# Optimization experiments

Hardware: AMD Instinct MI355X
Metric: run time of the kernel (lower is better)

Reference implementation:

```python
import jax, jax.numpy as jnp
import numpy as np

K = 20
EPS = 1e-5


def _knn_idx(pts, k):
    # pts: [B,N,C] -> [B,N,k] indices of k nearest neighbors (self included),
    # matching torch topk on negative squared distance.
    inner = jnp.einsum('bnc,bmc->bnm', pts, pts)
    sq = jnp.sum(pts * pts, axis=-1)
    neg_dist = 2.0 * inner - sq[:, :, None] - sq[:, None, :]  # [B,N,N]
    return jax.lax.top_k(neg_dist, k)[1]


def _graph_feature(pts, k):
    # pts: [B,N,C] -> edge features [B,N,k,2C] = concat(neighbor-center, center)
    idx = _knn_idx(pts, k)                       # [B,N,k]
    nb = jax.vmap(lambda p, i: p[i])(pts, idx)   # gather: [B,N,k,C]
    ctr = jnp.broadcast_to(pts[:, :, None, :], nb.shape)
    return jnp.concatenate([nb - ctr, ctr], axis=-1)


def _bn(x, g, b, axes):
    # BatchNorm with batch statistics (torch training-mode forward)
    m = jnp.mean(x, axes, keepdims=True)
    v = jnp.var(x, axes, keepdims=True)
    return (x - m) * jax.lax.rsqrt(v + EPS) * g + b


def _edge_block(pts, W, b, g, beta):
    # EdgeConv: graph feature -> 1x1 conv (matmul over channels) -> BN -> ReLU -> max over k
    f = _graph_feature(pts, K)                       # [B,N,k,2C]
    h = jnp.einsum('bnkc,oc->bnko', f, W) + b        # 1x1 conv
    h = jax.nn.relu(_bn(h, g, beta, (0, 1, 2)))
    return jnp.max(h, axis=2)                        # [B,N,O]


def _forward(x, conv1_w, conv1_b, bn1_g, bn1_b, conv2_w, conv2_b, bn2_g, bn2_b,
             conv3_w, conv3_b, bn3_g, bn3_b, conv4_w, conv4_b, bn4_g, bn4_b,
             fc1_w, fc1_b, bnf1_g, bnf1_b, fc2_w, fc2_b, bnf2_g, bnf2_b,
             fc3_w, fc3_b, bnf3_g, bnf3_b, fc4_w, fc4_b):
    pts = x[:, 0]  # squeeze(1): [B,N,3] (channels-last == torch [B,3,N] transposed)
    x1 = _edge_block(pts, conv1_w, conv1_b, bn1_g, bn1_b)   # [B,N,64]
    x2 = _edge_block(x1, conv2_w, conv2_b, bn2_g, bn2_b)    # [B,N,64]
    x3 = _edge_block(x2, conv3_w, conv3_b, bn3_g, bn3_b)    # [B,N,128]
    x4 = _edge_block(x3, conv4_w, conv4_b, bn4_g, bn4_b)    # [B,N,256]
    # maxpool over all N points (kernel (crop_point_num,1))
    x_64 = jnp.max(x2, axis=1)    # [B,64]
    x_128 = jnp.max(x3, axis=1)   # [B,128]
    x_256 = jnp.max(x4, axis=1)   # [B,256]
    h = jnp.concatenate([x_256, x_128, x_64], axis=1)  # [B,448]
    h = jax.nn.relu(_bn(h @ fc1_w.T + fc1_b, bnf1_g, bnf1_b, (0,)))
    h = jax.nn.relu(_bn(h @ fc2_w.T + fc2_b, bnf2_g, bnf2_b, (0,)))
    h = jax.nn.relu(_bn(h @ fc3_w.T + fc3_b, bnf3_g, bnf3_b, (0,)))
    return h @ fc4_w.T + fc4_b    # [B,1]


def setup_inputs() -> dict:
    key = jax.random.key(0)
    ks = jax.random.split(key, 16)
    B, N = 8, 2048
    f32 = jnp.float32

    def w(k, shape):
        return jax.random.normal(k, shape, f32) / np.float32(np.sqrt(shape[-1]))

    def bn_params(c):
        return jnp.ones((c,), f32), jnp.zeros((c,), f32)

    bn1_g, bn1_b = bn_params(64)
    bn2_g, bn2_b = bn_params(64)
    bn3_g, bn3_b = bn_params(128)
    bn4_g, bn4_b = bn_params(256)
    bnf1_g, bnf1_b = bn_params(256)
    bnf2_g, bnf2_b = bn_params(128)
    bnf3_g, bnf3_b = bn_params(16)
    return {
        'x': jax.random.normal(ks[0], (B, 1, N, 3), f32),
        'conv1_w': w(ks[1], (64, 6)),   'conv1_b': jnp.zeros((64,), f32),
        'bn1_g': bn1_g, 'bn1_b': bn1_b,
        'conv2_w': w(ks[2], (64, 128)), 'conv2_b': jnp.zeros((64,), f32),
        'bn2_g': bn2_g, 'bn2_b': bn2_b,
        'conv3_w': w(ks[3], (128, 128)), 'conv3_b': jnp.zeros((128,), f32),
        'bn3_g': bn3_g, 'bn3_b': bn3_b,
        'conv4_w': w(ks[4], (256, 256)), 'conv4_b': jnp.zeros((256,), f32),
        'bn4_g': bn4_g, 'bn4_b': bn4_b,
        'fc1_w': w(ks[5], (256, 448)), 'fc1_b': jnp.zeros((256,), f32),
        'bnf1_g': bnf1_g, 'bnf1_b': bnf1_b,
        'fc2_w': w(ks[6], (128, 256)), 'fc2_b': jnp.zeros((128,), f32),
        'bnf2_g': bnf2_g, 'bnf2_b': bnf2_b,
        'fc3_w': w(ks[7], (16, 128)), 'fc3_b': jnp.zeros((16,), f32),
        'bnf3_g': bnf3_g, 'bnf3_b': bnf3_b,
        'fc4_w': w(ks[8], (1, 16)), 'fc4_b': jnp.zeros((1,), f32),
    }


def reference(x, conv1_w, conv1_b, bn1_g, bn1_b, conv2_w, conv2_b, bn2_g, bn2_b,
              conv3_w, conv3_b, bn3_g, bn3_b, conv4_w, conv4_b, bn4_g, bn4_b,
              fc1_w, fc1_b, bnf1_g, bnf1_b, fc2_w, fc2_b, bnf2_g, bnf2_b,
              fc3_w, fc3_b, bnf3_g, bnf3_b, fc4_w, fc4_b):
    return _forward(x, conv1_w, conv1_b, bn1_g, bn1_b, conv2_w, conv2_b, bn2_g, bn2_b,
                    conv3_w, conv3_b, bn3_g, bn3_b, conv4_w, conv4_b, bn4_g, bn4_b,
                    fc1_w, fc1_b, bnf1_g, bnf1_b, fc2_w, fc2_b, bnf2_g, bnf2_b,
                    fc3_w, fc3_b, bnf3_g, bnf3_b, fc4_w, fc4_b)
```

## Files before the change

### kernel.cpp

```cpp
#include <hip/hip_runtime.h>
#include <hip/hip_bf16.h>
#include <cfloat>

constexpr int BATCH = 8, NPTS = 2048, KNN = 20;
constexpr int NROWS = BATCH * NPTS;
constexpr float EPSV = 1e-5f;
constexpr int SB = 256;
constexpr int PR = 64;
constexpr int RBB = NPTS / 16;
constexpr int KC2 = 48;
constexpr int QCAP = 512;
constexpr int NCH = 4;

using u16 = unsigned short;
using u64 = unsigned long long;
typedef __attribute__((ext_vector_type(8))) short short8;
typedef __attribute__((ext_vector_type(4))) float f32x4;

__global__ void diag_kernel(float* out, float v) {
    if (threadIdx.x < 8) out[threadIdx.x] = v;
}

__global__ __launch_bounds__(256) void fill_zero_kernel(float* __restrict__ p, int n) {
    int i = blockIdx.x * 256 + threadIdx.x;
    if (i < n) p[i] = 0.f;
}

template<int C>
__global__ __launch_bounds__(256) void sqnorm_kernel(const float* __restrict__ X,
                                                     float* __restrict__ sq) {
    int r = blockIdx.x * 256 + threadIdx.x;
    const float* x = X + (size_t)r * C;
    float s = 0.f;
#pragma unroll
    for (int c = 0; c < C; ++c) { float v = x[c]; s = fmaf(v, v, s); }
    sq[r] = s;
}

template<int C>
__global__ __launch_bounds__(256) void split_pack_kernel(const float* __restrict__ X,
                                                         u16* __restrict__ XPH,
                                                         u16* __restrict__ XPL) {
    constexpr int KB = C / 32;
    int e = blockIdx.x * 256 + threadIdx.x;
    int lane = e & 63;
    int rest = e >> 6;
    int kb = rest % KB;
    int Rb = rest / KB;
    int row = Rb * 16 + (lane & 15);
    int col = kb * 32 + (lane >> 4) * 8;
    const float* src = &X[(size_t)row * C + col];
    u16 h[8], l[8];
#pragma unroll
    for (int q = 0; q < 8; ++q) {
        float v = src[q];
        __hip_bfloat16 hb = __float2bfloat16(v);
        float hf = __bfloat162float(hb);
        __hip_bfloat16 lb = __float2bfloat16(v - hf);
        h[q] = *(u16*)&hb; l[q] = *(u16*)&lb;
    }
    u16* dh = &XPH[(size_t)e * 8];
    u16* dl = &XPL[(size_t)e * 8];
#pragma unroll
    for (int q = 0; q < 8; ++q) { dh[q] = h[q]; dl[q] = l[q]; }
}

template<int C, int O>
__global__ __launch_bounds__(256) void wsplit_pack_kernel(const float* __restrict__ W,
                                                          u16* __restrict__ WPH,
                                                          u16* __restrict__ WPL) {
    constexpr int KB = C / 32;
    constexpr int NFRAG = (2 * O / 16) * KB * 64;
    int e = blockIdx.x * 256 + threadIdx.x;
    if (e >= NFRAG) return;
    int lane = e & 63;
    int rest = e >> 6;
    int kb = rest % KB;
    int Nb = rest / KB;
    int n = Nb * 16 + (lane & 15);
    int col = kb * 32 + (lane >> 4) * 8;
    u16 h[8], l[8];
#pragma unroll
    for (int q = 0; q < 8; ++q) {
        int c = col + q;
        float wv = (n < O) ? W[(size_t)n * (2 * C) + c]
                           : W[(size_t)(n - O) * (2 * C) + C + c] - W[(size_t)(n - O) * (2 * C) + c];
        __hip_bfloat16 hb = __float2bfloat16(wv);
        float hf = __bfloat162float(hb);
        __hip_bfloat16 lb = __float2bfloat16(wv - hf);
        h[q] = *(u16*)&hb; l[q] = *(u16*)&lb;
    }
    u16* dh = &WPH[(size_t)e * 8];
    u16* dl = &WPL[(size_t)e * 8];
#pragma unroll
    for (int q = 0; q < 8; ++q) { dh[q] = h[q]; dl[q] = l[q]; }
}

__device__ __forceinline__ float bitonic64_desc_f32(float key, int lane) {
#pragma unroll
    for (int k = 2; k <= 64; k <<= 1) {
#pragma unroll
        for (int j = k >> 1; j > 0; j >>= 1) {
            float p = __shfl_xor(key, j);
            bool keepMax = (((lane & j) == 0) == ((lane & k) == 0));
            key = ((key > p) == keepMax) ? key : p;
        }
    }
    return key;
}

__device__ __forceinline__ u64 bitonic64_desc_u64(u64 key, int lane) {
#pragma unroll
    for (int k = 2; k <= 64; k <<= 1) {
#pragma unroll
        for (int j = k >> 1; j > 0; j >>= 1) {
            u64 p = __shfl_xor(key, j);
            bool keepMax = (((lane & j) == 0) == ((lane & k) == 0));
            key = ((key > p) == keepMax) ? key : p;
        }
    }
    return key;
}

template<int C>
__global__ __launch_bounds__(256) void dist_gemm_kernel(const float* __restrict__ X,
                                                        float* __restrict__ D, int b0) {
    constexpr int KC = (C < 32) ? C : 32;
    __shared__ __align__(16) float As[KC][68];
    __shared__ __align__(16) float Bs[KC][68];
    int b = b0 + blockIdx.z;
    int i0 = blockIdx.y * 64, j0 = blockIdx.x * 64;
    const float* Xb = X + (size_t)b * NPTS * C;
    int tx = threadIdx.x & 15, ty = threadIdx.x >> 4;
    float acc[4][4] = {};
    for (int c0 = 0; c0 < C; c0 += KC) {
        for (int t = threadIdx.x; t < 64 * KC; t += 256) {
            int i = t / KC, c = t % KC;
            As[c][i] = Xb[(size_t)(i0 + i) * C + c0 + c];
            Bs[c][i] = Xb[(size_t)(j0 + i) * C + c0 + c];
        }
        __syncthreads();
#pragma unroll
        for (int c = 0; c < KC; ++c) {
            const float4 av = *(const float4*)&As[c][ty * 4];
            const float4 bv = *(const float4*)&Bs[c][tx * 4];
            float ar[4] = {av.x, av.y, av.z, av.w};
            float br[4] = {bv.x, bv.y, bv.z, bv.w};
#pragma unroll
            for (int r = 0; r < 4; ++r)
#pragma unroll
                for (int q = 0; q < 4; ++q) acc[r][q] = fmaf(ar[r], br[q], acc[r][q]);
        }
        __syncthreads();
    }
    float* Dz = D + (size_t)blockIdx.z * NPTS * NPTS;
#pragma unroll
    for (int r = 0; r < 4; ++r) {
        float4 o4 = make_float4(acc[r][0], acc[r][1], acc[r][2], acc[r][3]);
        *(float4*)&Dz[(size_t)(i0 + ty * 4 + r) * NPTS + j0 + tx * 4] = o4;
    }
}

__global__ __launch_bounds__(256) void topk_kernel(const float* __restrict__ D,
                                                   const float* __restrict__ sq,
                                                   u16* __restrict__ idx_out, int b0) {
    __shared__ u64 qkey[4][QCAP];
    __shared__ int qn[4];
    int b = b0 + blockIdx.z;
    int w = threadIdx.x >> 6, lane = threadIdx.x & 63;
    int i = blockIdx.x * 4 + w;
    const float* Drow = D + ((size_t)blockIdx.z * NPTS + i) * NPTS;
    const float* sqb = sq + b * NPTS;
    float sqi = sqb[i];
    if (lane == 0) qn[w] = 0;

    float vals[32];
    float mx = -FLT_MAX;
#pragma unroll
    for (int t = 0; t < 8; ++t) {
        int j = t * 256 + lane * 4;
        float4 v4 = *(const float4*)&Drow[j];
        float4 s4 = *(const float4*)&sqb[j];
        float a0 = (2.f * v4.x - sqi - s4.x) + 0.f;
        float a1 = (2.f * v4.y - sqi - s4.y) + 0.f;
        float a2 = (2.f * v4.z - sqi - s4.z) + 0.f;
        float a3 = (2.f * v4.w - sqi - s4.w) + 0.f;
        vals[t * 4 + 0] = a0; vals[t * 4 + 1] = a1;
        vals[t * 4 + 2] = a2; vals[t * 4 + 3] = a3;
        mx = fmaxf(mx, fmaxf(fmaxf(a0, a1), fmaxf(a2, a3)));
    }

    float sm = bitonic64_desc_f32(mx, lane);
    float T0 = __shfl(sm, 19);

#pragma unroll
    for (int t = 0; t < 32; ++t) {
        float v = vals[t];
        if (v >= T0) {
            unsigned j = (unsigned)((t >> 2) * 256 + lane * 4 + (t & 3));
            unsigned bu = __float_as_uint(v);
            unsigned u = (bu & 0x80000000u) ? ~bu : (bu | 0x80000000u);
            u64 key = ((u64)u << 32) | (u64)(0xFFFFFFFFu - j);
            int slot = atomicAdd(&qn[w], 1);
            if (slot < QCAP) qkey[w][slot] = key;
        }
    }
    int C = qn[w];
    if (C > QCAP) C = QCAP;

    u64 key = (lane < C) ? qkey[w][lane] : 0ull;
    key = bitonic64_desc_u64(key, lane);
    int base = 64;
    while (base < C) {
        if (lane >= 20) {
            int src = base + (lane - 20);
            key = (src < C) ? qkey[w][src] : 0ull;
        }
        key = bitonic64_desc_u64(key, lane);
        base += 44;
    }
    if (lane < 20) {
        unsigned j = 0xFFFFFFFFu - (unsigned)(key & 0xFFFFFFFFull);
        idx_out[(size_t)(b * NPTS + i) * KNN + lane] = (u16)j;
    }
}

template<int C>
__global__ __launch_bounds__(256) void knn_kernel(const u16* __restrict__ XPH,
                                                  const u16* __restrict__ XPL,
                                                  const float* __restrict__ SQ,
                                                  u64* __restrict__ CAND) {
    constexpr int KB = C / 32;
    __shared__ float Dl[16][516];
    __shared__ u64 cand[16][KC2];
    __shared__ int cnt[16];
    int b = blockIdx.z;
    int chunk = blockIdx.x;
    int i0 = blockIdx.y * 16;
    int w = threadIdx.x >> 6, lane = threadIdx.x & 63;
    int l15 = lane & 15, g = lane >> 4;
    size_t base = (size_t)b * RBB * KB * 512;
    const float* sqb = SQ + b * NPTS;

    if (threadIdx.x < 16) cnt[threadIdx.x] = 0;

    int Rba = i0 / 16;
    short8 ahi[KB], alo[KB];
#pragma unroll
    for (int kb = 0; kb < KB; ++kb) {
        size_t ia = base + ((size_t)(Rba * KB + kb) * 64 + lane) * 8;
        ahi[kb] = *(const short8*)&XPH[ia];
        alo[kb] = *(const short8*)&XPL[ia];
    }
    float sqr[4];
#pragma unroll
    for (int r = 0; r < 4; ++r) sqr[r] = sqb[i0 + g * 4 + r];

#pragma unroll
    for (int t = 0; t < 8; ++t) {
        int c = w + 4 * t;
        int Cb = chunk * 32 + c;
        f32x4 acc = {0.f, 0.f, 0.f, 0.f};
#pragma unroll
        for (int kb = 0; kb < KB; ++kb) {
            size_t ib = base + ((size_t)(Cb * KB + kb) * 64 + lane) * 8;
            short8 bhi = *(const short8*)&XPH[ib];
            short8 blo = *(const short8*)&XPL[ib];
            acc = __builtin_amdgcn_mfma_f32_16x16x32_bf16(ahi[kb], bhi, acc, 0, 0, 0);
            acc = __builtin_amdgcn_mfma_f32_16x16x32_bf16(ahi[kb], blo, acc, 0, 0, 0);
            acc = __builtin_amdgcn_mfma_f32_16x16x32_bf16(alo[kb], bhi, acc, 0, 0, 0);
        }
        int colg = Cb * 16 + l15;
        float sqc = sqb[colg];
        int cl = c * 16 + l15;
#pragma unroll
        for (int r = 0; r < 4; ++r)
            Dl[g * 4 + r][cl] = (2.f * acc[r] - sqr[r] - sqc) + 0.f;
    }
    __syncthreads();

    for (int rr = 0; rr < 4; ++rr) {
        int row = w * 4 + rr;
        float vv[8];
        float mx = -FLT_MAX;
#pragma unroll
        for (int q = 0; q < 8; ++q) {
            vv[q] = Dl[row][lane + 64 * q];
            mx = fmaxf(mx, vv[q]);
        }
        float sv = bitonic64_desc_f32(mx, lane);
        float T = __shfl(sv, 19);
#pragma unroll
        for (int q = 0; q < 8; ++q) {
            float v = vv[q];
            if (v >= T) {
                unsigned colg = (unsigned)(chunk * 512 + lane + 64 * q);
                unsigned bu = __float_as_uint(v);
                unsigned u = (bu & 0x80000000u) ? ~bu : (bu | 0x80000000u);
                u64 key = ((u64)u << 32) | (u64)(0xFFFFFFFFu - colg);
                int slot = atomicAdd(&cnt[row], 1);
                if (slot < KC2) cand[row][slot] = key;
            }
        }
        int Cn = cnt[row]; if (Cn > KC2) Cn = KC2;
        u64 key = (lane < Cn) ? cand[row][lane] : 0ull;
        key = bitonic64_desc_u64(key, lane);
        if (lane < 20)
            CAND[(((size_t)(b * NPTS + i0 + row)) * NCH + chunk) * 20 + lane] = key;
    }
}

__global__ __launch_bounds__(256) void knn_merge_kernel(const u64* __restrict__ CAND,
                                                        u16* __restrict__ idx_out) {
    int b = blockIdx.z;
    int w = threadIdx.x >> 6, lane = threadIdx.x & 63;
    int i = blockIdx.x * 4 + w;
    size_t rb = ((size_t)(b * NPTS + i)) * (NCH * 20);
    u64 key = CAND[rb + lane];
    key = bitonic64_desc_u64(key, lane);
    u64 extra = (lane >= 20 && lane < 36) ? CAND[rb + 64 + (lane - 20)] : 0ull;
    if (lane >= 20) key = extra;
    key = bitonic64_desc_u64(key, lane);
    if (lane < 20) {
        unsigned j = 0xFFFFFFFFu - (unsigned)(key & 0xFFFFFFFFull);
        idx_out[((size_t)(b * NPTS + i)) * KNN + lane] = (u16)j;
    }
}

template<int C, int O>
__global__ __launch_bounds__(256) void uvb_mfma_kernel(const u16* __restrict__ XPH,
                                                       const u16* __restrict__ XPL,
                                                       const u16* __restrict__ WPH,
                                                       const u16* __restrict__ WPL,
                                                       const float* __restrict__ bias,
                                                       float* __restrict__ UVA) {
    constexpr int KB = C / 32;
    int b = blockIdx.z;
    int r0 = blockIdx.y * 64, n0 = blockIdx.x * 64;
    int w = threadIdx.x >> 6, lane = threadIdx.x & 63;
    int l15 = lane & 15, g = lane >> 4;
    size_t base = (size_t)b * RBB * KB * 512;
    int Rba = r0 / 16 + w;
    short8 ahi[KB], alo[KB];
#pragma unroll
    for (int kb = 0; kb < KB; ++kb) {
        size_t ia = base + ((size_t)(Rba * KB + kb) * 64 + lane) * 8;
        ahi[kb] = *(const short8*)&XPH[ia];
        alo[kb] = *(const short8*)&XPL[ia];
    }
    float* UVb = UVA + (size_t)b * NPTS * 2 * O;
#pragma unroll
    for (int nt = 0; nt < 4; ++nt) {
        int Nb = n0 / 16 + nt;
        f32x4 acc = {0.f, 0.f, 0.f, 0.f};
#pragma unroll
        for (int kb = 0; kb < KB; ++kb) {
            size_t ib = ((size_t)(Nb * KB + kb) * 64 + lane) * 8;
            short8 bhi = *(const short8*)&WPH[ib];
            short8 blo = *(const short8*)&WPL[ib];
            acc = __builtin_amdgcn_mfma_f32_16x16x32_bf16(ahi[kb], bhi, acc, 0, 0, 0);
            acc = __builtin_amdgcn_mfma_f32_16x16x32_bf16(ahi[kb], blo, acc, 0, 0, 0);
            acc = __builtin_amdgcn_mfma_f32_16x16x32_bf16(alo[kb], bhi, acc, 0, 0, 0);
        }
        int n = n0 + nt * 16 + l15;
        float badd = (n >= O) ? bias[n - O] : 0.f;
        int rbase = r0 + w * 16 + g * 4;
#pragma unroll
        for (int r = 0; r < 4; ++r)
            UVb[(size_t)(rbase + r) * (2 * O) + n] = acc[r] + badd;
    }
}

template<int C, int O>
__global__ __launch_bounds__(256) void uvb_gemm_kernel(const float* __restrict__ X,
                                                       const float* __restrict__ W,
                                                       const float* __restrict__ bias,
                                                       float* __restrict__ UVA) {
    constexpr int KC = (C < 32) ? C : 32;
    __shared__ __align__(16) float As[KC][68];
    __shared__ __align__(16) float Bs[KC][68];
    int b = blockIdx.z;
    int r0 = blockIdx.y * 64, n0 = blockIdx.x * 64;
    int tx = threadIdx.x & 15, ty = threadIdx.x >> 4;
    float acc[4][4] = {};
    for (int c0 = 0; c0 < C; c0 += KC) {
        for (int t = threadIdx.x; t < 64 * KC; t += 256) {
            int i = t / KC, c = t % KC;
            As[c][i] = X[(size_t)(b * NPTS + r0 + i) * C + c0 + c];
            int n = n0 + i;
            float wv;
            if (n < O) wv = W[(size_t)n * (2 * C) + c0 + c];
            else {
                int o = n - O;
                wv = W[(size_t)o * (2 * C) + C + c0 + c] - W[(size_t)o * (2 * C) + c0 + c];
            }
            Bs[c][i] = wv;
        }
        __syncthreads();
#pragma unroll
        for (int c = 0; c < KC; ++c) {
            const float4 av = *(const float4*)&As[c][ty * 4];
            const float4 bv = *(const float4*)&Bs[c][tx * 4];
            float ar[4] = {av.x, av.y, av.z, av.w};
            float br[4] = {bv.x, bv.y, bv.z, bv.w};
#pragma unroll
            for (int r = 0; r < 4; ++r)
#pragma unroll
                for (int q = 0; q < 4; ++q) acc[r][q] = fmaf(ar[r], br[q], acc[r][q]);
        }
        __syncthreads();
    }
    float badd[4] = {0.f, 0.f, 0.f, 0.f};
    if (n0 >= O) {
#pragma unroll
        for (int q = 0; q < 4; ++q) badd[q] = bias[n0 - O + tx * 4 + q];
    }
    float* UVb = UVA + (size_t)b * NPTS * 2 * O;
#pragma unroll
    for (int r = 0; r < 4; ++r) {
        float4 o4 = make_float4(acc[r][0] + badd[0], acc[r][1] + badd[1],
                                acc[r][2] + badd[2], acc[r][3] + badd[3]);
        *(float4*)&UVb[(size_t)(r0 + ty * 4 + r) * (2 * O) + n0 + tx * 4] = o4;
    }
}

template<int O>
__global__ __launch_bounds__(256) void statsb_kernel(const float* __restrict__ UVA,
                                                     const u16* __restrict__ idx,
                                                     float* __restrict__ PART,
                                                     float* __restrict__ HMAX,
                                                     float* __restrict__ HMIN) {
    constexpr int TPR = O / 4;
    constexpr int RPAR = 256 / TPR;
    constexpr int RPB = NPTS / SB;
    __shared__ float sh[256 * 8];
    int b = blockIdx.z;
    const float* UVb = UVA + (size_t)b * NPTS * 2 * O;
    int otid = threadIdx.x % TPR;
    int o = otid * 4;
    int rsub = threadIdx.x / TPR;
    int rbase = blockIdx.x * RPB;
    float s0 = 0, s1 = 0, s2 = 0, s3 = 0, q0 = 0, q1 = 0, q2 = 0, q3 = 0;
    for (int r = rbase + rsub; r < rbase + RPB; r += RPAR) {
        const float4 v4 = *(const float4*)&UVb[(size_t)r * (2 * O) + O + o];
        const u16* ix = idx + (size_t)(b * NPTS + r) * KNN;
        float mx0 = -FLT_MAX, mx1 = -FLT_MAX, mx2 = -FLT_MAX, mx3 = -FLT_MAX;
        float mn0 = FLT_MAX, mn1 = FLT_MAX, mn2 = FLT_MAX, mn3 = FLT_MAX;
#pragma unroll
        for (int k = 0; k < KNN; ++k) {
            int j = (int)ix[k] & (NPTS - 1);
            const float4 u4 = *(const float4*)&UVb[(size_t)j * (2 * O) + o];
            float h0 = u4.x + v4.x, h1 = u4.y + v4.y, h2 = u4.z + v4.z, h3 = u4.w + v4.w;
            s0 += h0; q0 = fmaf(h0, h0, q0); mx0 = fmaxf(mx0, h0); mn0 = fminf(mn0, h0);
            s1 += h1; q1 = fmaf(h1, h1, q1); mx1 = fmaxf(mx1, h1); mn1 = fminf(mn1, h1);
            s2 += h2; q2 = fmaf(h2, h2, q2); mx2 = fmaxf(mx2, h2); mn2 = fminf(mn2, h2);
            s3 += h3; q3 = fmaf(h3, h3, q3); mx3 = fmaxf(mx3, h3); mn3 = fminf(mn3, h3);
        }
        size_t R = (size_t)(b * NPTS + r) * O + o;
        *(float4*)&HMAX[R] = make_float4(mx0, mx1, mx2, mx3);
        *(float4*)&HMIN[R] = make_float4(mn0, mn1, mn2, mn3);
    }
    float* my = &sh[threadIdx.x * 8];
    my[0] = s0; my[1] = s1; my[2] = s2; my[3] = s3;
    my[4] = q0; my[5] = q1; my[6] = q2; my[7] = q3;
    __syncthreads();
    if (threadIdx.x < TPR) {
        float a[8];
#pragma unroll
        for (int c = 0; c < 8; ++c) a[c] = sh[threadIdx.x * 8 + c];
        for (int g = 1; g < RPAR; ++g) {
            const float* p = &sh[(g * TPR + threadIdx.x) * 8];
#pragma unroll
            for (int c = 0; c < 8; ++c) a[c] += p[c];
        }
        float* dst = &PART[((size_t)b * SB + blockIdx.x) * (2 * O)];
#pragma unroll
        for (int c = 0; c < 4; ++c) { dst[o + c] = a[c]; dst[O + o + c] = a[4 + c]; }
    }
}

template<int O>
__global__ __launch_bounds__(256) void part_reduce_kernel(const float* __restrict__ PART,
                                                          float* __restrict__ PART2) {
    constexpr int ROWS = BATCH * SB;
    constexpr int RPG = ROWS / PR;
    int g = blockIdx.x;
    for (int col = threadIdx.x; col < 2 * O; col += 256) {
        float s = 0.f;
        for (int r = 0; r < RPG; ++r)
            s += PART[(size_t)(g * RPG + r) * (2 * O) + col];
        PART2[(size_t)g * (2 * O) + col] = s;
    }
}

template<int O>
__global__ void bnp_kernel(const float* __restrict__ PART2, const float* __restrict__ g,
                           const float* __restrict__ beta, float* __restrict__ bnp) {
    int o = threadIdx.x;
    float s = 0.f, ss = 0.f;
    for (int p = 0; p < PR; ++p) {
        s += PART2[(size_t)p * (2 * O) + o];
        ss += PART2[(size_t)p * (2 * O) + O + o];
    }
    const float cnt = (float)NROWS * (float)KNN;
    float m = s / cnt;
    float var = ss / cnt - m * m;
    float sc = g[o] / sqrtf(var + EPSV);
    bnp[o] = sc;
    bnp[O + o] = beta[o] - m * sc;
}

template<int O>
__global__ __launch_bounds__(256) void applyb_kernel(const float* __restrict__ HMAX,
                                                     const float* __restrict__ HMIN,
                                                     const float* __restrict__ bnp,
                                                     float* __restrict__ Xn) {
    constexpr int TPR = O / 4;
    int e = blockIdx.x * 256 + threadIdx.x;
    int o = (e % TPR) * 4;
    size_t R = (size_t)(e / TPR) * O + o;
    const float4 hx = *(const float4*)&HMAX[R];
    const float4 hn = *(const float4*)&HMIN[R];
    float4 out;
    { float sc = bnp[o + 0], t = bnp[O + o + 0]; out.x = fmaxf(fmaf(sc, (sc >= 0.f) ? hx.x : hn.x, t), 0.f); }
    { float sc = bnp[o + 1], t = bnp[O + o + 1]; out.y = fmaxf(fmaf(sc, (sc >= 0.f) ? hx.y : hn.y, t), 0.f); }
    { float sc = bnp[o + 2], t = bnp[O + o + 2]; out.z = fmaxf(fmaf(sc, (sc >= 0.f) ? hx.z : hn.z, t), 0.f); }
    { float sc = bnp[o + 3], t = bnp[O + o + 3]; out.w = fmaxf(fmaf(sc, (sc >= 0.f) ? hx.w : hn.w, t), 0.f); }
    *(float4*)&Xn[R] = out;
}

__global__ __launch_bounds__(256) void applyb4_kernel(const float* __restrict__ HMAX,
                                                      const float* __restrict__ HMIN,
                                                      const float* __restrict__ bnp,
                                                      float* __restrict__ g0T) {
    constexpr int O = 256;
    constexpr int TPR = O / 4;
    constexpr int RPAR = 256 / TPR;
    constexpr int AB = 32;
    constexpr int RPB = NPTS / AB;
    __shared__ float sh[256 * 4];
    int b = blockIdx.z;
    int otid = threadIdx.x & (TPR - 1);
    int o = otid * 4;
    int rsub = threadIdx.x >> 6;
    int rbase = blockIdx.x * RPB;
    float sc0 = bnp[o + 0], t0 = bnp[O + o + 0];
    float sc1 = bnp[o + 1], t1 = bnp[O + o + 1];
    float sc2 = bnp[o + 2], t2 = bnp[O + o + 2];
    float sc3 = bnp[o + 3], t3 = bnp[O + o + 3];
    float ym0 = 0.f, ym1 = 0.f, ym2 = 0.f, ym3 = 0.f;
    for (int r = rbase + rsub; r < rbase + RPB; r += RPAR) {
        size_t R = (size_t)(b * NPTS + r) * O + o;
        const float4 hx = *(const float4*)&HMAX[R];
        const float4 hn = *(const float4*)&HMIN[R];
        ym0 = fmaxf(ym0, fmaf(sc0, (sc0 >= 0.f) ? hx.x : hn.x, t0));
        ym1 = fmaxf(ym1, fmaf(sc1, (sc1 >= 0.f) ? hx.y : hn.y, t1));
        ym2 = fmaxf(ym2, fmaf(sc2, (sc2 >= 0.f) ? hx.z : hn.z, t2));
        ym3 = fmaxf(ym3, fmaf(sc3, (sc3 >= 0.f) ? hx.w : hn.w, t3));
    }
    float* my = &sh[threadIdx.x * 4];
    my[0] = ym0; my[1] = ym1; my[2] = ym2; my[3] = ym3;
    __syncthreads();
    if (threadIdx.x < TPR) {
        float a0 = ym0, a1 = ym1, a2 = ym2, a3 = ym3;
        for (int g = 1; g < RPAR; ++g) {
            const float* p = &sh[(g * TPR + threadIdx.x) * 4];
            a0 = fmaxf(a0, p[0]); a1 = fmaxf(a1, p[1]);
            a2 = fmaxf(a2, p[2]); a3 = fmaxf(a3, p[3]);
        }
        a0 = fmaxf(a0, 0.f); a1 = fmaxf(a1, 0.f);
        a2 = fmaxf(a2, 0.f); a3 = fmaxf(a3, 0.f);
        atomicMax((int*)&g0T[(o + 0) * 8 + b], __float_as_int(a0));
        atomicMax((int*)&g0T[(o + 1) * 8 + b], __float_as_int(a1));
        atomicMax((int*)&g0T[(o + 2) * 8 + b], __float_as_int(a2));
        atomicMax((int*)&g0T[(o + 3) * 8 + b], __float_as_int(a3));
    }
}

__global__ __launch_bounds__(256) void gmax23_kernel(const float* __restrict__ X2,
                                                     const float* __restrict__ X3,
                                                     float* __restrict__ g0T) {
    int b = blockIdx.x;
    int n0 = blockIdx.y * 32;
    int o = threadIdx.x;
    if (o >= 192) return;
    const float* src; int col, stride, ch;
    if (o < 128) { src = X3; col = o;       stride = 128; ch = 256 + o; }
    else         { src = X2; col = o - 128; stride = 64;  ch = 384 + (o - 128); }
    float m = 0.f;
#pragma unroll 8
    for (int n = n0; n < n0 + 32; ++n)
        m = fmaxf(m, src[((size_t)(b * NPTS + n)) * stride + col]);
    atomicMax((int*)&g0T[ch * 8 + b], __float_as_int(m));
}

__global__ __launch_bounds__(256) void transpose_kernel(const float* __restrict__ w,
                                                        float* __restrict__ wT, int O, int Cc) {
    int e = blockIdx.x * 256 + threadIdx.x;
    if (e >= O * Cc) return;
    int o = e / Cc, c = e - o * Cc;
    wT[c * O + o] = w[e];
}

__global__ __launch_bounds__(64) void fc1_kernel(const float* __restrict__ g0T,
                                                 const float* __restrict__ w1T,
                                                 const float* __restrict__ b1,
                                                 const float* __restrict__ bng,
                                                 const float* __restrict__ bnb,
                                                 float* __restrict__ A) {
    int o = blockIdx.x * 64 + threadIdx.x;
    float acc[8] = {};
    for (int c = 0; c < 448; ++c) {
        float wv = w1T[c * 256 + o];
        const float4 h0 = *(const float4*)&g0T[c * 8];
        const float4 h1 = *(const float4*)&g0T[c * 8 + 4];
        acc[0] = fmaf(wv, h0.x, acc[0]); acc[1] = fmaf(wv, h0.y, acc[1]);
        acc[2] = fmaf(wv, h0.z, acc[2]); acc[3] = fmaf(wv, h0.w, acc[3]);
        acc[4] = fmaf(wv, h1.x, acc[4]); acc[5] = fmaf(wv, h1.y, acc[5]);
        acc[6] = fmaf(wv, h1.z, acc[6]); acc[7] = fmaf(wv, h1.w, acc[7]);
    }
    float bb = b1[o];
    float h[8], m = 0.f;
#pragma unroll
    for (int b = 0; b < 8; ++b) { h[b] = acc[b] + bb; m += h[b]; }
    m *= 0.125f;
    float var = 0.f;
#pragma unroll
    for (int b = 0; b < 8; ++b) { float d = h[b] - m; var = fmaf(d, d, var); }
    var *= 0.125f;
    float sc = bng[o] / sqrtf(var + EPSV);
    float t = bnb[o] - m * sc;
#pragma unroll
    for (int b = 0; b < 8; ++b) A[o * 8 + b] = fmaxf(fmaf(sc, h[b], t), 0.f);
}

__global__ __launch_bounds__(256) void tail_kernel(const float* __restrict__ A,
                                                   const float* __restrict__ w2T, const float* __restrict__ b2,
                                                   const float* __restrict__ g2, const float* __restrict__ be2,
                                                   const float* __restrict__ w3T, const float* __restrict__ b3,
                                                   const float* __restrict__ g3, const float* __restrict__ be3,
                                                   const float* __restrict__ w4, const float* __restrict__ b4,
                                                   float* __restrict__ out) {
    __shared__ __align__(16) float B2[128 * 8];
    __shared__ __align__(16) float C3[16 * 8];
    int tid = threadIdx.x;
    if (tid < 128) {
        int o = tid;
        float acc[8] = {};
        for (int c = 0; c < 256; ++c) {
            float wv = w2T[c * 128 + o];
            const float4 a0 = *(const float4*)&A[c * 8];
            const float4 a1 = *(const float4*)&A[c * 8 + 4];
            acc[0] = fmaf(wv, a0.x, acc[0]); acc[1] = fmaf(wv, a0.y, acc[1]);
            acc[2] = fmaf(wv, a0.z, acc[2]); acc[3] = fmaf(wv, a0.w, acc[3]);
            acc[4] = fmaf(wv, a1.x, acc[4]); acc[5] = fmaf(wv, a1.y, acc[5]);
            acc[6] = fmaf(wv, a1.z, acc[6]); acc[7] = fmaf(wv, a1.w, acc[7]);
        }
        float bb = b2[o];
        float h[8], m = 0.f;
#pragma unroll
        for (int b = 0; b < 8; ++b) { h[b] = acc[b] + bb; m += h[b]; }
        m *= 0.125f;
        float var = 0.f;
#pragma unroll
        for (int b = 0; b < 8; ++b) { float d = h[b] - m; var = fmaf(d, d, var); }
        var *= 0.125f;
        float sc = g2[o] / sqrtf(var + EPSV);
        float t = be2[o] - m * sc;
#pragma unroll
        for (int b = 0; b < 8; ++b) B2[o * 8 + b] = fmaxf(fmaf(sc, h[b], t), 0.f);
    }
    __syncthreads();
    if (tid < 16) {
        int o = tid;
        float acc[8] = {};
        for (int c = 0; c < 128; ++c) {
            float wv = w3T[c * 16 + o];
            const float4 a0 = *(const float4*)&B2[c * 8];
            const float4 a1 = *(const float4*)&B2[c * 8 + 4];
            acc[0] = fmaf(wv, a0.x, acc[0]); acc[1] = fmaf(wv, a0.y, acc[1]);
            acc[2] = fmaf(wv, a0.z, acc[2]); acc[3] = fmaf(wv, a0.w, acc[3]);
            acc[4] = fmaf(wv, a1.x, acc[4]); acc[5] = fmaf(wv, a1.y, acc[5]);
            acc[6] = fmaf(wv, a1.z, acc[6]); acc[7] = fmaf(wv, a1.w, acc[7]);
        }
        float bb = b3[o];
        float h[8], m = 0.f;
#pragma unroll
        for (int b = 0; b < 8; ++b) { h[b] = acc[b] + bb; m += h[b]; }
        m *= 0.125f;
        float var = 0.f;
#pragma unroll
        for (int b = 0; b < 8; ++b) { float d = h[b] - m; var = fmaf(d, d, var); }
        var *= 0.125f;
        float sc = g3[o] / sqrtf(var + EPSV);
        float t = be3[o] - m * sc;
#pragma unroll
        for (int b = 0; b < 8; ++b) C3[o * 8 + b] = fmaxf(fmaf(sc, h[b], t), 0.f);
    }
    __syncthreads();
    if (tid < 8) {
        int b = tid;
        float acc = b4[0];
#pragma unroll
        for (int c = 0; c < 16; ++c) acc = fmaf(w4[c], C3[c * 8 + b], acc);
        out[b] = acc;
    }
}

struct Arena {
    char* base; size_t off, cap; bool ok;
    Arena(void* b, size_t c) : base((char*)b), off(0), cap(c), ok(true) {}
    void* get(size_t bytes) {
        char* p = base + off;
        off += (bytes + 255) & ~(size_t)255;
        if (off > cap) ok = false;
        return p;
    }
};

template<int C, int O>
static void run_stage(const float* Xin, float* Xout, const float* W, const float* bias,
                      const float* g, const float* be, float* SCRBIG, float* UVA,
                      u16* XPH, u16* XPL, u16* WPH, u16* WPL,
                      u16* IDX, float* SQ, float* PART, float* PART2, float* BNP, hipStream_t s) {
    dim3 blk(256);
    float* HMAX = SCRBIG;
    float* HMIN = SCRBIG + (size_t)NROWS * O;
    u64* CANDB = (u64*)SCRBIG;
    sqnorm_kernel<C><<<NROWS / 256, blk, 0, s>>>(Xin, SQ);
    if constexpr (C >= 32) {
        split_pack_kernel<C><<<NROWS * C / 8 / 256, blk, 0, s>>>(Xin, XPH, XPL);
        knn_kernel<C><<<dim3(NCH, NPTS / 16, BATCH), blk, 0, s>>>(XPH, XPL, SQ, CANDB);
        knn_merge_kernel<<<dim3(NPTS / 4, 1, BATCH), blk, 0, s>>>(CANDB, IDX);
        wsplit_pack_kernel<C, O><<<(2 * O * C / 8 + 255) / 256, blk, 0, s>>>(W, WPH, WPL);
        uvb_mfma_kernel<C, O><<<dim3(2 * O / 64, NPTS / 64, BATCH), blk, 0, s>>>(XPH, XPL, WPH, WPL, bias, UVA);
    } else {
        for (int b0 = 0; b0 < BATCH; b0 += 4) {
            dist_gemm_kernel<C><<<dim3(NPTS / 64, NPTS / 64, 4), blk, 0, s>>>(Xin, SCRBIG, b0);
            topk_kernel<<<dim3(NPTS / 4, 1, 4), blk, 0, s>>>(SCRBIG, SQ, IDX, b0);
        }
        uvb_gemm_kernel<C, O><<<dim3(2 * O / 64, NPTS / 64, BATCH), blk, 0, s>>>(Xin, W, bias, UVA);
    }
    statsb_kernel<O><<<dim3(SB, 1, BATCH), blk, 0, s>>>(UVA, IDX, PART, HMAX, HMIN);
    part_reduce_kernel<O><<<PR, blk, 0, s>>>(PART, PART2);
    bnp_kernel<O><<<1, O, 0, s>>>(PART2, g, be, BNP);
    applyb_kernel<O><<<NROWS * (O / 4) / 256, blk, 0, s>>>(HMAX, HMIN, BNP, Xout);
}

static void run_stage4(const float* Xin, const float* W, const float* bias,
                       const float* g, const float* be, float* SCRBIG, float* UVA,
                       u16* XPH, u16* XPL, u16* WPH, u16* WPL,
                       u16* IDX, float* SQ, float* PART, float* PART2, float* BNP, float* G0T,
                       hipStream_t s) {
    constexpr int C = 128;
    dim3 blk(256);
    float* HMAX = SCRBIG;
    float* HMIN = SCRBIG + (size_t)NROWS * 256;
    u64* CANDB = (u64*)SCRBIG;
    sqnorm_kernel<C><<<NROWS / 256, blk, 0, s>>>(Xin, SQ);
    split_pack_kernel<C><<<NROWS * C / 8 / 256, blk, 0, s>>>(Xin, XPH, XPL);
    knn_kernel<C><<<dim3(NCH, NPTS / 16, BATCH), blk, 0, s>>>(XPH, XPL, SQ, CANDB);
    knn_merge_kernel<<<dim3(NPTS / 4, 1, BATCH), blk, 0, s>>>(CANDB, IDX);
    wsplit_pack_kernel<C, 256><<<(512 * C / 8 + 255) / 256, blk, 0, s>>>(W, WPH, WPL);
    uvb_mfma_kernel<C, 256><<<dim3(8, NPTS / 64, BATCH), blk, 0, s>>>(XPH, XPL, WPH, WPL, bias, UVA);
    statsb_kernel<256><<<dim3(SB, 1, BATCH), blk, 0, s>>>(UVA, IDX, PART, HMAX, HMIN);
    part_reduce_kernel<256><<<PR, blk, 0, s>>>(PART, PART2);
    bnp_kernel<256><<<1, 256, 0, s>>>(PART2, g, be, BNP);
    fill_zero_kernel<<<14, blk, 0, s>>>(G0T, 448 * 8);
    applyb4_kernel<<<dim3(32, 1, BATCH), blk, 0, s>>>(HMAX, HMIN, BNP, G0T);
}

extern "C" void kernel_launch(void* const* d_in, const int* in_sizes, int n_in,
                              void* d_out, int out_size, void* d_ws, size_t ws_size,
                              hipStream_t stream) {
    float* out = (float*)d_out;
    if (n_in < 31) { diag_kernel<<<1, 64, 0, stream>>>(out, 9000.f); return; }

    const float* x       = (const float*)d_in[0];
    const float* cw[4]   = {(const float*)d_in[1], (const float*)d_in[5], (const float*)d_in[9],  (const float*)d_in[13]};
    const float* cb[4]   = {(const float*)d_in[2], (const float*)d_in[6], (const float*)d_in[10], (const float*)d_in[14]};
    const float* bg[4]   = {(const float*)d_in[3], (const float*)d_in[7], (const float*)d_in[11], (const float*)d_in[15]};
    const float* bb[4]   = {(const float*)d_in[4], (const float*)d_in[8], (const float*)d_in[12], (const float*)d_in[16]};
    const float* fc1_w = (const float*)d_in[17]; const float* fc1_b = (const float*)d_in[18];
    const float* bnf1_g = (const float*)d_in[19]; const float* bnf1_b = (const float*)d_in[20];
    const float* fc2_w = (const float*)d_in[21]; const float* fc2_b = (const float*)d_in[22];
    const float* bnf2_g = (const float*)d_in[23]; const float* bnf2_b = (const float*)d_in[24];
    const float* fc3_w = (const float*)d_in[25]; const float* fc3_b = (const float*)d_in[26];
    const float* bnf3_g = (const float*)d_in[27]; const float* bnf3_b = (const float*)d_in[28];
    const float* fc4_w = (const float*)d_in[29]; const float* fc4_b = (const float*)d_in[30];

    Arena ar(d_ws, ws_size);
    float* X1 = (float*)ar.get((size_t)NROWS * 64 * 4);
    float* X2 = (float*)ar.get((size_t)NROWS * 64 * 4);
    float* X3 = (float*)ar.get((size_t)NROWS * 128 * 4);
    u16* IDX = (u16*)ar.get((size_t)NROWS * KNN * 2);
    float* SQ = (float*)ar.get((size_t)NROWS * 4);
    float* PART = (float*)ar.get((size_t)BATCH * SB * 512 * 4);
    float* PART2 = (float*)ar.get((size_t)PR * 512 * 4);
    float* BNP = (float*)ar.get(512 * 4);
    float* G0T = (float*)ar.get(448 * 8 * 4);
    float* ABUF = (float*)ar.get(256 * 8 * 4);
    u16* XPH = (u16*)ar.get((size_t)NROWS * 128 * 2);
    u16* XPL = (u16*)ar.get((size_t)NROWS * 128 * 2);
    u16* WPH = (u16*)ar.get(512 * 128 * 2);
    u16* WPL = (u16*)ar.get(512 * 128 * 2);
    float* SCRBIG = (float*)ar.get((size_t)4 * NPTS * NPTS * 4);
    if (!ar.ok) {
        diag_kernel<<<1, 64, 0, stream>>>(out, 3000.f + (float)(ws_size >> 20));
        return;
    }
    float* UVA = SCRBIG + (size_t)2 * NPTS * NPTS;

    dim3 blk(256);
    run_stage<3, 64>(x, X1, cw[0], cb[0], bg[0], bb[0], SCRBIG, UVA, XPH, XPL, WPH, WPL, IDX, SQ, PART, PART2, BNP, stream);
    run_stage<64, 64>(X1, X2, cw[1], cb[1], bg[1], bb[1], SCRBIG, UVA, XPH, XPL, WPH, WPL, IDX, SQ, PART, PART2, BNP, stream);
    run_stage<64, 128>(X2, X3, cw[2], cb[2], bg[2], bb[2], SCRBIG, UVA, XPH, XPL, WPH, WPL, IDX, SQ, PART, PART2, BNP, stream);
    run_stage4(X3, cw[3], cb[3], bg[3], bb[3], SCRBIG, UVA, XPH, XPL, WPH, WPL, IDX, SQ, PART, PART2, BNP, G0T, stream);

    gmax23_kernel<<<dim3(BATCH, 64), blk, 0, stream>>>(X2, X3, G0T);

    float* W1T = SCRBIG;
    float* W2T = W1T + 448 * 256;
    float* W3T = W2T + 256 * 128;
    transpose_kernel<<<(256 * 448 + 255) / 256, blk, 0, stream>>>(fc1_w, W1T, 256, 448);
    transpose_kernel<<<(128 * 256 + 255) / 256, blk, 0, stream>>>(fc2_w, W2T, 128, 256);
    transpose_kernel<<<(16 * 128 + 255) / 256, blk, 0, stream>>>(fc3_w, W3T, 16, 128);
    fc1_kernel<<<4, 64, 0, stream>>>(G0T, W1T, fc1_b, bnf1_g, bnf1_b, ABUF);
    tail_kernel<<<1, 256, 0, stream>>>(ABUF, W2T, fc2_b, bnf2_g, bnf2_b,
                                       W3T, fc3_b, bnf3_g, bnf3_b, fc4_w, fc4_b, out);
}
```

Measured before the change: 718.2 us.

## Fuse stage-1 distance GEMM with top-k and move kNN candidate sorting into merge

For the 3-channel first stage, the separate distance GEMM and top-k kernels are replaced by one kernel. It stages the batch's points and squared norms in shared memory and computes distances on the fly, so the 4×2048×2048 distance matrix is no longer written to and read back from global memory. In the MFMA kNN kernel, candidates above the per-chunk threshold are compacted with ballot/popcount and written straight to global memory with per-chunk counts, instead of being sorted locally through shared-memory atomics; the merge kernel now streams the variable-length lists through bitonic sorts. Risks: the fused kernel caps candidates at 64 where the old one allowed 512, so heavy ties could drop true neighbours, and every block reloads all 2048 points of its batch.

```diff
diff --git a/kernel.cpp b/kernel.cpp
--- a/kernel.cpp
+++ b/kernel.cpp
@@ -9,7 +9,6 @@
 constexpr int PR = 64;
 constexpr int RBB = NPTS / 16;
 constexpr int KC2 = 48;
-constexpr int QCAP = 512;
 constexpr int NCH = 4;
 
 using u16 = unsigned short;
@@ -122,106 +121,57 @@
     return key;
 }
 
-template<int C>
-__global__ __launch_bounds__(256) void dist_gemm_kernel(const float* __restrict__ X,
-                                                        float* __restrict__ D, int b0) {
-    constexpr int KC = (C < 32) ? C : 32;
-    __shared__ __align__(16) float As[KC][68];
-    __shared__ __align__(16) float Bs[KC][68];
-    int b = b0 + blockIdx.z;
-    int i0 = blockIdx.y * 64, j0 = blockIdx.x * 64;
-    const float* Xb = X + (size_t)b * NPTS * C;
-    int tx = threadIdx.x & 15, ty = threadIdx.x >> 4;
-    float acc[4][4] = {};
-    for (int c0 = 0; c0 < C; c0 += KC) {
-        for (int t = threadIdx.x; t < 64 * KC; t += 256) {
-            int i = t / KC, c = t % KC;
-            As[c][i] = Xb[(size_t)(i0 + i) * C + c0 + c];
-            Bs[c][i] = Xb[(size_t)(j0 + i) * C + c0 + c];
-        }
-        __syncthreads();
-#pragma unroll
-        for (int c = 0; c < KC; ++c) {
-            const float4 av = *(const float4*)&As[c][ty * 4];
-            const float4 bv = *(const float4*)&Bs[c][tx * 4];
-            float ar[4] = {av.x, av.y, av.z, av.w};
-            float br[4] = {bv.x, bv.y, bv.z, bv.w};
-#pragma unroll
-            for (int r = 0; r < 4; ++r)
-#pragma unroll
-                for (int q = 0; q < 4; ++q) acc[r][q] = fmaf(ar[r], br[q], acc[r][q]);
-        }
-        __syncthreads();
-    }
-    float* Dz = D + (size_t)blockIdx.z * NPTS * NPTS;
-#pragma unroll
-    for (int r = 0; r < 4; ++r) {
-        float4 o4 = make_float4(acc[r][0], acc[r][1], acc[r][2], acc[r][3]);
-        *(float4*)&Dz[(size_t)(i0 + ty * 4 + r) * NPTS + j0 + tx * 4] = o4;
-    }
-}
-
-__global__ __launch_bounds__(256) void topk_kernel(const float* __restrict__ D,
-                                                   const float* __restrict__ sq,
-                                                   u16* __restrict__ idx_out, int b0) {
-    __shared__ u64 qkey[4][QCAP];
+__global__ __launch_bounds__(256) void topk1_kernel(const float* __restrict__ X,
+                                                    u16* __restrict__ idx_out) {
+    constexpr int Q1 = 64;
+    __shared__ float px[NPTS], py[NPTS], pz[NPTS], sqs[NPTS];
+    __shared__ u64 qkey[4][Q1];
     __shared__ int qn[4];
-    int b = b0 + blockIdx.z;
+    int b = blockIdx.z;
+    const float* Xb = X + (size_t)b * NPTS * 3;
+    for (int k = threadIdx.x; k < NPTS; k += 256) {
+        float xx = Xb[k * 3 + 0], yy = Xb[k * 3 + 1], zz = Xb[k * 3 + 2];
+        px[k] = xx; py[k] = yy; pz[k] = zz;
+        float s = fmaf(xx, xx, 0.f); s = fmaf(yy, yy, s); s = fmaf(zz, zz, s);
+        sqs[k] = s;
+    }
     int w = threadIdx.x >> 6, lane = threadIdx.x & 63;
+    if (lane == 0) qn[w] = 0;
+    __syncthreads();
     int i = blockIdx.x * 4 + w;
-    const float* Drow = D + ((size_t)blockIdx.z * NPTS + i) * NPTS;
-    const float* sqb = sq + b * NPTS;
-    float sqi = sqb[i];
-    if (lane == 0) qn[w] = 0;
-
+    float xi = px[i], yi = py[i], zi = pz[i], sqi = sqs[i];
     float vals[32];
     float mx = -FLT_MAX;
 #pragma unroll
-    for (int t = 0; t < 8; ++t) {
-        int j = t * 256 + lane * 4;
-        float4 v4 = *(const float4*)&Drow[j];
-        float4 s4 = *(const float4*)&sqb[j];
-        float a0 = (2.f * v4.x - sqi - s4.x) + 0.f;
-        float a1 = (2.f * v4.y - sqi - s4.y) + 0.f;
-        float a2 = (2.f * v4.z - sqi - s4.z) + 0.f;
-        float a3 = (2.f * v4.w - sqi - s4.w) + 0.f;
-        vals[t * 4 + 0] = a0; vals[t * 4 + 1] = a1;
-        vals[t * 4 + 2] = a2; vals[t * 4 + 3] = a3;
-        mx = fmaxf(mx, fmaxf(fmaxf(a0, a1), fmaxf(a2, a3)));
-    }
-
+    for (int t = 0; t < 32; ++t) {
+        int j = lane + 64 * t;
+        float d = fmaf(xi, px[j], 0.f);
+        d = fmaf(yi, py[j], d);
+        d = fmaf(zi, pz[j], d);
+        float v = (2.f * d - sqi - sqs[j]) + 0.f;
+        vals[t] = v;
+        mx = fmaxf(mx, v);
+    }
     float sm = bitonic64_desc_f32(mx, lane);
     float T0 = __shfl(sm, 19);
-
 #pragma unroll
     for (int t = 0; t < 32; ++t) {
         float v = vals[t];
         if (v >= T0) {
-            unsigned j = (unsigned)((t >> 2) * 256 + lane * 4 + (t & 3));
+            unsigned j = (unsigned)(lane + 64 * t);
             unsigned bu = __float_as_uint(v);
             unsigned u = (bu & 0x80000000u) ? ~bu : (bu | 0x80000000u);
             u64 key = ((u64)u << 32) | (u64)(0xFFFFFFFFu - j);
             int slot = atomicAdd(&qn[w], 1);
-            if (slot < QCAP) qkey[w][slot] = key;
-        }
-    }
-    int C = qn[w];
-    if (C > QCAP) C = QCAP;
-
-    u64 key = (lane < C) ? qkey[w][lane] : 0ull;
+            if (slot < Q1) qkey[w][slot] = key;
+        }
+    }
+    int Cn = qn[w]; if (Cn > Q1) Cn = Q1;
+    u64 key = (lane < Cn) ? qkey[w][lane] : 0ull;
     key = bitonic64_desc_u64(key, lane);
-    int base = 64;
-    while (base < C) {
-        if (lane >= 20) {
-            int src = base + (lane - 20);
-            key = (src < C) ? qkey[w][src] : 0ull;
-        }
-        key = bitonic64_desc_u64(key, lane);
-        base += 44;
-    }
     if (lane < 20) {
         unsigned j = 0xFFFFFFFFu - (unsigned)(key & 0xFFFFFFFFull);
-        idx_out[(size_t)(b * NPTS + i) * KNN + lane] = (u16)j;
+        idx_out[((size_t)(b * NPTS + i)) * KNN + lane] = (u16)j;
     }
 }
 
@@ -229,11 +179,10 @@
 __global__ __launch_bounds__(256) void knn_kernel(const u16* __restrict__ XPH,
                                                   const u16* __restrict__ XPL,
                                                   const float* __restrict__ SQ,
-                                                  u64* __restrict__ CAND) {
+                                                  u64* __restrict__ CAND,
+                                                  int* __restrict__ CNTS) {
     constexpr int KB = C / 32;
     __shared__ float Dl[16][516];
-    __shared__ u64 cand[16][KC2];
-    __shared__ int cnt[16];
     int b = blockIdx.z;
     int chunk = blockIdx.x;
     int i0 = blockIdx.y * 16;
@@ -242,8 +191,6 @@
     size_t base = (size_t)b * RBB * KB * 512;
     const float* sqb = SQ + b * NPTS;
 
-    if (threadIdx.x < 16) cnt[threadIdx.x] = 0;
-
     int Rba = i0 / 16;
     short8 ahi[KB], alo[KB];
 #pragma unroll
@@ -290,40 +237,55 @@
         }
         float sv = bitonic64_desc_f32(mx, lane);
         float T = __shfl(sv, 19);
+        size_t cb = ((size_t)(b * NPTS + i0 + row) * NCH + chunk) * KC2;
+        int cbase = 0;
 #pragma unroll
         for (int q = 0; q < 8; ++q) {
-            float v = vv[q];
-            if (v >= T) {
-                unsigned colg = (unsigned)(chunk * 512 + lane + 64 * q);
-                unsigned bu = __float_as_uint(v);
-                unsigned u = (bu & 0x80000000u) ? ~bu : (bu | 0x80000000u);
-                u64 key = ((u64)u << 32) | (u64)(0xFFFFFFFFu - colg);
-                int slot = atomicAdd(&cnt[row], 1);
-                if (slot < KC2) cand[row][slot] = key;
+            bool p = vv[q] >= T;
+            u64 mask = __ballot(p);
+            int ofs = __popcll(mask & ((1ull << lane) - 1ull));
+            if (p) {
+                int slot = cbase + ofs;
+                if (slot < KC2) {
+                    unsigned colg = (unsigned)(chunk * 512 + lane + 64 * q);
+                    unsigned bu = __float_as_uint(vv[q]);
+                    unsigned u = (bu & 0x80000000u) ? ~bu : (bu | 0x80000000u);
+                    CAND[cb + slot] = ((u64)u << 32) | (u64)(0xFFFFFFFFu - colg);
+                }
             }
-        }
-        int Cn = cnt[row]; if (Cn > KC2) Cn = KC2;
-        u64 key = (lane < Cn) ? cand[row][lane] : 0ull;
-        key = bitonic64_desc_u64(key, lane);
-        if (lane < 20)
-            CAND[(((size_t)(b * NPTS + i0 + row)) * NCH + chunk) * 20 + lane] = key;
+            cbase += __popcll(mask);
+        }
+        if (lane == 0)
+            CNTS[(size_t)(b * NPTS + i0 + row) * NCH + chunk] = (cbase < KC2) ? cbase : KC2;
     }
 }
 
 __global__ __launch_bounds__(256) void knn_merge_kernel(const u64* __restrict__ CAND,
+                                                        const int* __restrict__ CNTS,
                                                         u16* __restrict__ idx_out) {
     int b = blockIdx.z;
     int w = threadIdx.x >> 6, lane = threadIdx.x & 63;
     int i = blockIdx.x * 4 + w;
-    size_t rb = ((size_t)(b * NPTS + i)) * (NCH * 20);
-    u64 key = CAND[rb + lane];
+    size_t rbase = (size_t)(b * NPTS + i) * NCH;
+    int c0 = CNTS[rbase + 0];
+    u64 key = (lane < c0) ? CAND[(rbase + 0) * KC2 + lane] : 0ull;
     key = bitonic64_desc_u64(key, lane);
-    u64 extra = (lane >= 20 && lane < 36) ? CAND[rb + 64 + (lane - 20)] : 0ull;
-    if (lane >= 20) key = extra;
-    key = bitonic64_desc_u64(key, lane);
+    for (int ch = 1; ch < NCH; ++ch) {
+        int cn = CNTS[rbase + ch];
+        int off = 0;
+        while (off < cn) {
+            int take = cn - off; if (take > 44) take = 44;
+            if (lane >= 20) {
+                int s2 = lane - 20;
+                key = (s2 < take) ? CAND[(rbase + ch) * KC2 + off + s2] : 0ull;
+            }
+            key = bitonic64_desc_u64(key, lane);
+            off += take;
+        }
+    }
     if (lane < 20) {
         unsigned j = 0xFFFFFFFFu - (unsigned)(key & 0xFFFFFFFFull);
-        idx_out[((size_t)(b * NPTS + i)) * KNN + lane] = (u16)j;
+        idx_out[(size_t)(b * NPTS + i) * KNN + lane] = (u16)j;
     }
 }
 
@@ -727,18 +689,16 @@
     float* HMAX = SCRBIG;
     float* HMIN = SCRBIG + (size_t)NROWS * O;
     u64* CANDB = (u64*)SCRBIG;
-    sqnorm_kernel<C><<<NROWS / 256, blk, 0, s>>>(Xin, SQ);
+    int* CNTS = (int*)(CANDB + (size_t)NROWS * NCH * KC2);
     if constexpr (C >= 32) {
+        sqnorm_kernel<C><<<NROWS / 256, blk, 0, s>>>(Xin, SQ);
         split_pack_kernel<C><<<NROWS * C / 8 / 256, blk, 0, s>>>(Xin, XPH, XPL);
-        knn_kernel<C><<<dim3(NCH, NPTS / 16, BATCH), blk, 0, s>>>(XPH, XPL, SQ, CANDB);
-        knn_merge_kernel<<<dim3(NPTS / 4, 1, BATCH), blk, 0, s>>>(CANDB, IDX);
+        knn_kernel<C><<<dim3(NCH, NPTS / 16, BATCH), blk, 0, s>>>(XPH, XPL, SQ, CANDB, CNTS);
+        knn_merge_kernel<<<dim3(NPTS / 4, 1, BATCH), blk, 0, s>>>(CANDB, CNTS, IDX);
         wsplit_pack_kernel<C, O><<<(2 * O * C / 8 + 255) / 256, blk, 0, s>>>(W, WPH, WPL);
         uvb_mfma_kernel<C, O><<<dim3(2 * O / 64, NPTS / 64, BATCH), blk, 0, s>>>(XPH, XPL, WPH, WPL, bias, UVA);
     } else {
-        for (int b0 = 0; b0 < BATCH; b0 += 4) {
-            dist_gemm_kernel<C><<<dim3(NPTS / 64, NPTS / 64, 4), blk, 0, s>>>(Xin, SCRBIG, b0);
-            topk_kernel<<<dim3(NPTS / 4, 1, 4), blk, 0, s>>>(SCRBIG, SQ, IDX, b0);
-        }
+        topk1_kernel<<<dim3(NPTS / 4, 1, BATCH), blk, 0, s>>>(Xin, IDX);
         uvb_gemm_kernel<C, O><<<dim3(2 * O / 64, NPTS / 64, BATCH), blk, 0, s>>>(Xin, W, bias, UVA);
     }
     statsb_kernel<O><<<dim3(SB, 1, BATCH), blk, 0, s>>>(UVA, IDX, PART, HMAX, HMIN);
@@ -757,10 +717,11 @@
     float* HMAX = SCRBIG;
     float* HMIN = SCRBIG + (size_t)NROWS * 256;
     u64* CANDB = (u64*)SCRBIG;
+    int* CNTS = (int*)(CANDB + (size_t)NROWS * NCH * KC2);
     sqnorm_kernel<C><<<NROWS / 256, blk, 0, s>>>(Xin, SQ);
     split_pack_kernel<C><<<NROWS * C / 8 / 256, blk, 0, s>>>(Xin, XPH, XPL);
-    knn_kernel<C><<<dim3(NCH, NPTS / 16, BATCH), blk, 0, s>>>(XPH, XPL, SQ, CANDB);
-    knn_merge_kernel<<<dim3(NPTS / 4, 1, BATCH), blk, 0, s>>>(CANDB, IDX);
+    knn_kernel<C><<<dim3(NCH, NPTS / 16, BATCH), blk, 0, s>>>(XPH, XPL, SQ, CANDB, CNTS);
+    knn_merge_kernel<<<dim3(NPTS / 4, 1, BATCH), blk, 0, s>>>(CANDB, CNTS, IDX);
     wsplit_pack_kernel<C, 256><<<(512 * C / 8 + 255) / 256, blk, 0, s>>>(W, WPH, WPL);
     uvb_mfma_kernel<C, 256><<<dim3(8, NPTS / 64, BATCH), blk, 0, s>>>(XPH, XPL, WPH, WPL, bias, UVA);
     statsb_kernel<256><<<dim3(SB, 1, BATCH), blk, 0, s>>>(UVA, IDX, PART, HMAX, HMIN);
```

Measured after the change: 660.4 us. -8.1%, faster.
